# Kernel tuning notes

Measured on AMD Instinct MI355X. Metric: run time of the kernel, lower is better.

The kernel has to match this reference:

```python
import jax, jax.numpy as jnp
import numpy as np

N_NODES = 100000
D = 128
R = 4          # number of edge types
E = 500000     # edges per relation


def setup_inputs() -> dict:
    key = jax.random.key(0)
    ks = jax.random.split(key, 6)
    x = jax.random.normal(ks[0], (N_NODES, D), dtype=jnp.float32)
    src = jax.random.randint(ks[1], (R, E), 0, N_NODES)
    dst = jax.random.randint(ks[2], (R, E), 0, N_NODES)
    # Per-relation SAGEConv (mean) parameters: fc_self, fc_neigh, bias
    scale = 1.0 / np.sqrt(D)
    Wself = jax.random.normal(ks[3], (R, D, D), dtype=jnp.float32) * scale
    Wneigh = jax.random.normal(ks[4], (R, D, D), dtype=jnp.float32) * scale
    b = jnp.zeros((R, D), dtype=jnp.float32)
    return {"x": x, "src": src, "dst": dst, "Wself": Wself, "Wneigh": Wneigh, "b": b}


def reference(x, src, dst, Wself, Wneigh, b):
    """HetGraphLayer with SAGE(mean) convs per relation + mean channel combine.

    x:     [N, D] node features (same node set for all relations)
    src:   [R, E] int source node ids per relation
    dst:   [R, E] int destination node ids per relation
    Wself, Wneigh: [R, D, D]; b: [R, D]
    """
    N = x.shape[0]

    def one_relation(s, d, Ws, Wn, bb):
        msg = x[s]                                                   # [E, D] gather
        summed = jax.ops.segment_sum(msg, d, num_segments=N)         # [N, D] scatter-add
        cnt = jax.ops.segment_sum(jnp.ones(s.shape, x.dtype), d, num_segments=N)
        neigh = summed / jnp.maximum(cnt, 1.0)[:, None]              # mean aggregation
        return x @ Ws + neigh @ Wn + bb                              # SAGEConv(mean)

    rel_embs = jax.vmap(one_relation)(src, dst, Wself, Wneigh, b)    # [R, N, D]
    # ChannelCombine('mean'): average across relation channels
    return rel_embs.mean(axis=0)                                     # [N, D]
```

## Files before the change

### kernel.cpp

```cpp
#include <hip/hip_runtime.h>
#include <hip/hip_bf16.h>
#include <stdint.h>

#define N_NODES 100000
#define DIM 128
#define NREL 4
#define NEDGE 500000
#define M_FLAT (NREL * N_NODES)
#define TOT_E (NREL * NEDGE)
#define BSLOT 1024
#define NBK ((M_FLAT + BSLOT - 1) / BSLOT)
#define CAP 8192
#define CHUNK 4096

typedef __attribute__((ext_vector_type(8))) short short8;
typedef __attribute__((ext_vector_type(4))) float f32x4;
typedef __attribute__((ext_vector_type(2))) float f32x2;

__device__ __forceinline__ unsigned short f2bf(float f) {
  unsigned int u = __float_as_uint(f);
  u += 0x7fffu + ((u >> 16) & 1u);
  return (unsigned short)(u >> 16);
}

__global__ void prep_kernel(const float* __restrict__ Ws, const float* __restrict__ Wn,
                            const float* __restrict__ bv, unsigned short* __restrict__ Wt,
                            float* __restrict__ biasc) {
  int tid = blockIdx.x * 256 + threadIdx.x;
  if (tid < 5 * DIM * DIM) {
    int b = tid / (DIM * DIM);
    int idx = tid - b * DIM * DIM;
    int k = idx >> 7, n = idx & 127;
    float v;
    if (b == 0)
      v = 0.25f * (Ws[idx] + Ws[DIM * DIM + idx] + Ws[2 * DIM * DIM + idx] + Ws[3 * DIM * DIM + idx]);
    else
      v = 0.25f * Wn[(b - 1) * DIM * DIM + idx];
    int ks = k >> 5, kq = (k >> 3) & 3, j = k & 7;
    int ct = n >> 4, lr = n & 15;
    int lane = kq * 16 + lr;
    Wt[((((b * 4 + ks) * 8) + ct) * 64 + lane) * 8 + j] = f2bf(v);
  }
  if (tid < DIM)
    biasc[tid] = 0.25f * (bv[tid] + bv[DIM + tid] + bv[2 * DIM + tid] + bv[3 * DIM + tid]);
}

__global__ void xb_kernel(const float* __restrict__ x, unsigned short* __restrict__ xb) {
  int i = blockIdx.x * 256 + threadIdx.x;
  if (i < N_NODES * DIM / 4) {
    float4 v = ((const float4*)x)[i];
    ushort4 s;
    s.x = f2bf(v.x); s.y = f2bf(v.y); s.z = f2bf(v.z); s.w = f2bf(v.w);
    ((ushort4*)xb)[i] = s;
  }
}

__global__ __launch_bounds__(256) void bscatter_kernel(
    const int* __restrict__ src, const int* __restrict__ dst,
    int* __restrict__ bcnt, unsigned int* __restrict__ gpairs) {
  __shared__ unsigned int buf[CHUNK];
  __shared__ unsigned short barr[CHUNK];
  __shared__ int hist[NBK];
  __shared__ int sbase[NBK];
  __shared__ int lcur[NBK];
  __shared__ int gbase[NBK];
  __shared__ int part[256];
  int tid = threadIdx.x;
  int base = blockIdx.x * CHUNK;
  int m = TOT_E - base; if (m > CHUNK) m = CHUNK;
  for (int i = tid; i < NBK; i += 256) { hist[i] = 0; lcur[i] = 0; }
  __syncthreads();
  unsigned int pk[CHUNK / 256];
  int bk[CHUNK / 256];
#pragma unroll
  for (int k = 0; k < CHUNK / 256; ++k) {
    int i = k * 256 + tid;
    int idx = base + i;
    int b = -1; unsigned int p = 0;
    if (i < m) {
      int r = idx / NEDGE;
      int fl = r * N_NODES + dst[idx];
      b = fl >> 10;
      p = ((unsigned int)(fl & (BSLOT - 1)) << 17) | (unsigned int)src[idx];
      atomicAdd(&hist[b], 1);
    }
    pk[k] = p; bk[k] = b;
  }
  __syncthreads();
  {
    int vA = hist[tid];
    part[tid] = vA;
    __syncthreads();
    for (int o = 1; o < 256; o <<= 1) {
      int u = (tid >= o) ? part[tid - o] : 0;
      __syncthreads();
      part[tid] += u;
      __syncthreads();
    }
    sbase[tid] = part[tid] - vA;
    int totalA = part[255];
    __syncthreads();
    int vB = (256 + tid < NBK) ? hist[256 + tid] : 0;
    part[tid] = vB;
    __syncthreads();
    for (int o = 1; o < 256; o <<= 1) {
      int u = (tid >= o) ? part[tid - o] : 0;
      __syncthreads();
      part[tid] += u;
      __syncthreads();
    }
    if (256 + tid < NBK) sbase[256 + tid] = totalA + part[tid] - vB;
  }
  __syncthreads();
#pragma unroll
  for (int k = 0; k < CHUNK / 256; ++k) {
    if (bk[k] >= 0) {
      int pos = sbase[bk[k]] + atomicAdd(&lcur[bk[k]], 1);
      buf[pos] = pk[k];
      barr[pos] = (unsigned short)bk[k];
    }
  }
  __syncthreads();
  for (int i = tid; i < NBK; i += 256)
    if (hist[i] > 0) gbase[i] = i * CAP + atomicAdd(&bcnt[i], hist[i]) - sbase[i];
  __syncthreads();
  for (int j = tid; j < m; j += 256)
    gpairs[gbase[barr[j]] + j] = buf[j];
}

__global__ __launch_bounds__(256) void bfill_kernel(
    const unsigned int* __restrict__ gpairs, const int* __restrict__ bcnt,
    int* __restrict__ offs, int* __restrict__ ssrc) {
  __shared__ int lcnt[BSLOT];
  __shared__ int lofs[BSLOT];
  __shared__ int lcur[BSLOT];
  __shared__ int part[256];
  int b = blockIdx.x;
  int tid = threadIdx.x;
  int base = b * CAP;
  int cntb = bcnt[b];
  int flBase = b << 10;
  int flCount = M_FLAT - flBase; if (flCount > BSLOT) flCount = BSLOT;
  for (int i = tid; i < BSLOT; i += 256) { lcnt[i] = 0; lcur[i] = 0; }
  __syncthreads();
  for (int j = tid; j < cntb; j += 256)
    atomicAdd(&lcnt[gpairs[base + j] >> 17], 1);
  __syncthreads();
  int vals[4]; int s0 = 0;
#pragma unroll
  for (int k = 0; k < 4; ++k) { vals[k] = lcnt[tid * 4 + k]; s0 += vals[k]; }
  part[tid] = s0;
  __syncthreads();
  for (int o = 1; o < 256; o <<= 1) {
    int u = (tid >= o) ? part[tid - o] : 0;
    __syncthreads();
    part[tid] += u;
    __syncthreads();
  }
  int excl = part[tid] - s0;
#pragma unroll
  for (int k = 0; k < 4; ++k) { lofs[tid * 4 + k] = excl; excl += vals[k]; }
  __syncthreads();
  for (int i = tid; i <= flCount; i += 256)
    offs[b * (BSLOT + 1) + i] = base + ((i < BSLOT) ? lofs[i] : cntb);
  for (int j = tid; j < cntb; j += 256) {
    unsigned int p = gpairs[base + j];
    int li = p >> 17;
    int pos = atomicAdd(&lcur[li], 1);
    ssrc[base + lofs[li] + pos] = (int)(p & 0x1FFFFu);
  }
}

__global__ __launch_bounds__(256) void aggregate_kernel(
    const unsigned int* __restrict__ xb32, const int* __restrict__ ssrc,
    const int* __restrict__ offs, unsigned int* __restrict__ agg32) {
  int lane = threadIdx.x & 63;
  int n = blockIdx.x * 4 + (int)__builtin_amdgcn_readfirstlane(threadIdx.x >> 6);
  if (n >= N_NODES) return;

  int start[NREL], end[NREL];
#pragma unroll
  for (int r = 0; r < NREL; ++r) {
    int fl = r * N_NODES + n;
    int oidx = fl + (fl >> 10);
    start[r] = __builtin_amdgcn_readfirstlane(offs[oidx]);
    end[r] = __builtin_amdgcn_readfirstlane(offs[oidx + 1]);
  }

  unsigned int v[NREL][8];
#pragma unroll
  for (int r = 0; r < NREL; ++r) {
    int s = start[r], m = end[r] - s;
#pragma unroll
    for (int k = 0; k < 8; ++k) {
      int ea = (m > 0) ? (s + ((k < m) ? k : (m - 1))) : 0;
      int idx = ssrc[ea];
      v[r][k] = xb32[((unsigned)idx << 6) | (unsigned)lane];
    }
  }

  f32x2 acc[NREL];
#pragma unroll
  for (int r = 0; r < NREL; ++r) {
    f32x2 a = {0.f, 0.f};
    int m = end[r] - start[r];
#pragma unroll
    for (int k = 0; k < 8; ++k) {
      unsigned int u = (k < m) ? v[r][k] : 0u;
      f32x2 d;
      d.x = __uint_as_float(u << 16);
      d.y = __uint_as_float(u & 0xffff0000u);
      a += d;
    }
    acc[r] = a;
  }

  bool anyTail = ((end[0] - start[0]) > 8) | ((end[1] - start[1]) > 8) |
                 ((end[2] - start[2]) > 8) | ((end[3] - start[3]) > 8);
  if (anyTail) {
#pragma unroll
    for (int r = 0; r < NREL; ++r) {
      for (int e = start[r] + 8; e < end[r]; e += 8) {
        int m = end[r] - e;
        unsigned int w[8];
#pragma unroll
        for (int k = 0; k < 8; ++k) {
          int idx = ssrc[e + ((k < m) ? k : 0)];
          w[k] = xb32[((unsigned)idx << 6) | (unsigned)lane];
        }
#pragma unroll
        for (int k = 0; k < 8; ++k) {
          unsigned int u = (k < m) ? w[k] : 0u;
          f32x2 d;
          d.x = __uint_as_float(u << 16);
          d.y = __uint_as_float(u & 0xffff0000u);
          acc[r] += d;
        }
      }
    }
  }

#pragma unroll
  for (int r = 0; r < NREL; ++r) {
    int c = end[r] - start[r];
    float inv = __builtin_amdgcn_rcpf((float)(c > 0 ? c : 1));
    float lo = acc[r].x * inv, hi = acc[r].y * inv;
    unsigned int packed;
    asm("v_cvt_pk_bf16_f32 %0, %1, %2" : "=v"(packed) : "v"(lo), "v"(hi));
    agg32[((size_t)r * N_NODES + n) * 64 + lane] = packed;
  }
}

__global__ __launch_bounds__(256) void gemm_kernel(
    const unsigned short* __restrict__ xb, const unsigned short* __restrict__ Wt,
    const float* __restrict__ biasc, float* __restrict__ out,
    const unsigned short* __restrict__ agg, int slabBase, int bLo, int bHi, int accum) {
  __shared__ short8 Bs[2048];
  int tid = threadIdx.x;
  int lane = tid & 63;
  int wv = __builtin_amdgcn_readfirstlane(tid >> 6);
  int bandRow = blockIdx.x * 128 + wv * 32;
  int valid = bandRow < N_NODES;
  int ldRow = valid ? bandRow : 0;
  int quad = lane >> 4;
  int lr = lane & 15;
  const short8* Bp = (const short8*)Wt;

  float bias8[8];
#pragma unroll
  for (int ct = 0; ct < 8; ++ct) bias8[ct] = biasc[ct * 16 + lr];

  f32x4 zero = {0.f, 0.f, 0.f, 0.f};
  f32x4 acc[2][8];
#pragma unroll
  for (int rt = 0; rt < 2; ++rt)
#pragma unroll
    for (int ct = 0; ct < 8; ++ct) acc[rt][ct] = zero;

#pragma unroll
  for (int p = 0; p < 8; ++p) Bs[p * 256 + tid] = Bp[(size_t)bLo * 2048 + p * 256 + tid];
  __syncthreads();

  for (int bi = bLo; bi <= bHi; ++bi) {
    const unsigned short* as =
        (bi == 0) ? xb : agg + (size_t)(bi - 1 - slabBase) * N_NODES * DIM;
    const unsigned short* rowp = as + (size_t)(ldRow + lr) * DIM;
    short8 a0[4], a1[4];
#pragma unroll
    for (int ks = 0; ks < 4; ++ks) {
      int k0 = ks * 32 + quad * 8;
      a0[ks] = *(const short8*)(rowp + k0);
      a1[ks] = *(const short8*)(rowp + 16 * DIM + k0);
    }
#pragma unroll
    for (int ks = 0; ks < 4; ++ks) {
#pragma unroll
      for (int ct = 0; ct < 8; ++ct) {
        short8 bf = Bs[(ks * 8 + ct) * 64 + lane];
        acc[0][ct] = __builtin_amdgcn_mfma_f32_16x16x32_bf16(a0[ks], bf, acc[0][ct], 0, 0, 0);
        acc[1][ct] = __builtin_amdgcn_mfma_f32_16x16x32_bf16(a1[ks], bf, acc[1][ct], 0, 0, 0);
      }
    }
    if (bi < bHi) {
      __syncthreads();
#pragma unroll
      for (int p = 0; p < 8; ++p)
        Bs[p * 256 + tid] = Bp[(size_t)(bi + 1) * 2048 + p * 256 + tid];
      __syncthreads();
    }
  }

  if (valid) {
#pragma unroll
    for (int rt = 0; rt < 2; ++rt)
#pragma unroll
      for (int i = 0; i < 4; ++i) {
        int g = bandRow + rt * 16 + quad * 4 + i;
        if (accum == 0) {
#pragma unroll
          for (int ct = 0; ct < 8; ++ct)
            out[(size_t)g * DIM + ct * 16 + lr] = acc[rt][ct][i] + bias8[ct];
        } else {
#pragma unroll
          for (int ct = 0; ct < 8; ++ct)
            out[(size_t)g * DIM + ct * 16 + lr] += acc[rt][ct][i];
        }
      }
  }
}

extern "C" void kernel_launch(void* const* d_in, const int* in_sizes, int n_in,
                              void* d_out, int out_size, void* d_ws, size_t ws_size,
                              hipStream_t stream) {
  const float* x = (const float*)d_in[0];
  const int* src = (const int*)d_in[1];
  const int* dst = (const int*)d_in[2];
  const float* Wself = (const float*)d_in[3];
  const float* Wneigh = (const float*)d_in[4];
  const float* bv = (const float*)d_in[5];
  float* out = (float*)d_out;

  char* ws = (char*)d_ws;
  size_t off = 0;
  int* bcnt = (int*)(ws + off);        off += 2048;
  unsigned short* Wt = (unsigned short*)(ws + off);  off += 5 * DIM * DIM * 2;
  float* biasc = (float*)(ws + off);   off += DIM * 4;
  int* offs = (int*)(ws + off);        off += ((size_t)NBK * (BSLOT + 1) * 4 + 15) & ~15;
  unsigned short* xb = (unsigned short*)(ws + off);  off += (size_t)N_NODES * DIM * 2;
  unsigned int* gpairs = (unsigned int*)(ws + off);  off += (size_t)NBK * CAP * 4;
  int* ssrc = (int*)(ws + off);        off += (size_t)NBK * CAP * 4;
  unsigned short* agg = (unsigned short*)(ws + off);

  hipMemsetAsync(bcnt, 0, 2048, stream);
  xb_kernel<<<(N_NODES * DIM / 4 + 255) / 256, 256, 0, stream>>>(x, xb);
  prep_kernel<<<(5 * DIM * DIM + 255) / 256, 256, 0, stream>>>(Wself, Wneigh, bv, Wt, biasc);
  bscatter_kernel<<<(TOT_E + CHUNK - 1) / CHUNK, 256, 0, stream>>>(src, dst, bcnt, gpairs);
  bfill_kernel<<<NBK, 256, 0, stream>>>(gpairs, bcnt, offs, ssrc);

  int gAgg = (N_NODES + 3) / 4;
  aggregate_kernel<<<gAgg, 256, 0, stream>>>((const unsigned int*)xb, ssrc, offs,
                                             (unsigned int*)agg);
  gemm_kernel<<<(N_NODES + 127) / 128, 256, 0, stream>>>(xb, Wt, biasc, out, agg,
                                                         0, 0, NREL, 0);
}
```

Measured before the change: 304.2 us.

## Fuse preprocessing kernels into one launch and prefetch A tiles in GEMM

Merges the bf16 conversion of x, the weight/bias prep and the edge bucket-scatter into a single block-partitioned kernel, cutting two launches and letting the independent work run concurrently. The scatter chunk size is doubled, which halves the scatter block count but raises shared memory and register use per block. The conversion path now batches eight float4 loads per thread. The GEMM is specialised to a fixed five-slab loop that loads the next slab's A rows while the current slab's MFMAs run.

New measurement: 295.1 us. 3.0% less time.

```diff
diff --git a/kernel.cpp b/kernel.cpp
--- a/kernel.cpp
+++ b/kernel.cpp
@@ -11,7 +11,12 @@
 #define BSLOT 1024
 #define NBK ((M_FLAT + BSLOT - 1) / BSLOT)
 #define CAP 8192
-#define CHUNK 4096
+#define CHUNK 8192
+#define NBSC ((TOT_E + CHUNK - 1) / CHUNK)
+#define NQ (N_NODES * DIM / 4)
+#define XB_BATCH 8
+#define NBXB ((NQ + 256 * XB_BATCH - 1) / (256 * XB_BATCH))
+#define NBPREP ((5 * DIM * DIM + 255) / 256)
 
 typedef __attribute__((ext_vector_type(8))) short short8;
 typedef __attribute__((ext_vector_type(4))) float f32x4;
@@ -23,41 +28,13 @@
   return (unsigned short)(u >> 16);
 }
 
-__global__ void prep_kernel(const float* __restrict__ Ws, const float* __restrict__ Wn,
-                            const float* __restrict__ bv, unsigned short* __restrict__ Wt,
-                            float* __restrict__ biasc) {
-  int tid = blockIdx.x * 256 + threadIdx.x;
-  if (tid < 5 * DIM * DIM) {
-    int b = tid / (DIM * DIM);
-    int idx = tid - b * DIM * DIM;
-    int k = idx >> 7, n = idx & 127;
-    float v;
-    if (b == 0)
-      v = 0.25f * (Ws[idx] + Ws[DIM * DIM + idx] + Ws[2 * DIM * DIM + idx] + Ws[3 * DIM * DIM + idx]);
-    else
-      v = 0.25f * Wn[(b - 1) * DIM * DIM + idx];
-    int ks = k >> 5, kq = (k >> 3) & 3, j = k & 7;
-    int ct = n >> 4, lr = n & 15;
-    int lane = kq * 16 + lr;
-    Wt[((((b * 4 + ks) * 8) + ct) * 64 + lane) * 8 + j] = f2bf(v);
-  }
-  if (tid < DIM)
-    biasc[tid] = 0.25f * (bv[tid] + bv[DIM + tid] + bv[2 * DIM + tid] + bv[3 * DIM + tid]);
-}
-
-__global__ void xb_kernel(const float* __restrict__ x, unsigned short* __restrict__ xb) {
-  int i = blockIdx.x * 256 + threadIdx.x;
-  if (i < N_NODES * DIM / 4) {
-    float4 v = ((const float4*)x)[i];
-    ushort4 s;
-    s.x = f2bf(v.x); s.y = f2bf(v.y); s.z = f2bf(v.z); s.w = f2bf(v.w);
-    ((ushort4*)xb)[i] = s;
-  }
-}
-
-__global__ __launch_bounds__(256) void bscatter_kernel(
+__global__ __launch_bounds__(256) void pre_kernel(
     const int* __restrict__ src, const int* __restrict__ dst,
-    int* __restrict__ bcnt, unsigned int* __restrict__ gpairs) {
+    int* __restrict__ bcnt, unsigned int* __restrict__ gpairs,
+    const float* __restrict__ x, unsigned short* __restrict__ xb,
+    const float* __restrict__ Ws, const float* __restrict__ Wn,
+    const float* __restrict__ bv, unsigned short* __restrict__ Wt,
+    float* __restrict__ biasc) {
   __shared__ unsigned int buf[CHUNK];
   __shared__ unsigned short barr[CHUNK];
   __shared__ int hist[NBK];
@@ -65,67 +42,106 @@
   __shared__ int lcur[NBK];
   __shared__ int gbase[NBK];
   __shared__ int part[256];
+  int bid = blockIdx.x;
   int tid = threadIdx.x;
-  int base = blockIdx.x * CHUNK;
-  int m = TOT_E - base; if (m > CHUNK) m = CHUNK;
-  for (int i = tid; i < NBK; i += 256) { hist[i] = 0; lcur[i] = 0; }
-  __syncthreads();
-  unsigned int pk[CHUNK / 256];
-  int bk[CHUNK / 256];
-#pragma unroll
-  for (int k = 0; k < CHUNK / 256; ++k) {
-    int i = k * 256 + tid;
-    int idx = base + i;
-    int b = -1; unsigned int p = 0;
-    if (i < m) {
-      int r = idx / NEDGE;
-      int fl = r * N_NODES + dst[idx];
-      b = fl >> 10;
-      p = ((unsigned int)(fl & (BSLOT - 1)) << 17) | (unsigned int)src[idx];
-      atomicAdd(&hist[b], 1);
-    }
-    pk[k] = p; bk[k] = b;
-  }
-  __syncthreads();
-  {
-    int vA = hist[tid];
-    part[tid] = vA;
-    __syncthreads();
-    for (int o = 1; o < 256; o <<= 1) {
-      int u = (tid >= o) ? part[tid - o] : 0;
-      __syncthreads();
-      part[tid] += u;
-      __syncthreads();
-    }
-    sbase[tid] = part[tid] - vA;
-    int totalA = part[255];
-    __syncthreads();
-    int vB = (256 + tid < NBK) ? hist[256 + tid] : 0;
-    part[tid] = vB;
-    __syncthreads();
-    for (int o = 1; o < 256; o <<= 1) {
-      int u = (tid >= o) ? part[tid - o] : 0;
-      __syncthreads();
-      part[tid] += u;
-      __syncthreads();
-    }
-    if (256 + tid < NBK) sbase[256 + tid] = totalA + part[tid] - vB;
-  }
-  __syncthreads();
-#pragma unroll
-  for (int k = 0; k < CHUNK / 256; ++k) {
-    if (bk[k] >= 0) {
-      int pos = sbase[bk[k]] + atomicAdd(&lcur[bk[k]], 1);
-      buf[pos] = pk[k];
-      barr[pos] = (unsigned short)bk[k];
-    }
-  }
-  __syncthreads();
-  for (int i = tid; i < NBK; i += 256)
-    if (hist[i] > 0) gbase[i] = i * CAP + atomicAdd(&bcnt[i], hist[i]) - sbase[i];
-  __syncthreads();
-  for (int j = tid; j < m; j += 256)
-    gpairs[gbase[barr[j]] + j] = buf[j];
+
+  if (bid < NBSC) {
+    int base = bid * CHUNK;
+    int m = TOT_E - base; if (m > CHUNK) m = CHUNK;
+    for (int i = tid; i < NBK; i += 256) { hist[i] = 0; lcur[i] = 0; }
+    __syncthreads();
+    unsigned int pk[CHUNK / 256];
+    int bk[CHUNK / 256];
+#pragma unroll
+    for (int k = 0; k < CHUNK / 256; ++k) {
+      int i = k * 256 + tid;
+      int idx = base + i;
+      int b = -1; unsigned int p = 0;
+      if (i < m) {
+        int r = idx / NEDGE;
+        int fl = r * N_NODES + dst[idx];
+        b = fl >> 10;
+        p = ((unsigned int)(fl & (BSLOT - 1)) << 17) | (unsigned int)src[idx];
+        atomicAdd(&hist[b], 1);
+      }
+      pk[k] = p; bk[k] = b;
+    }
+    __syncthreads();
+    {
+      int vA = hist[tid];
+      part[tid] = vA;
+      __syncthreads();
+      for (int o = 1; o < 256; o <<= 1) {
+        int u = (tid >= o) ? part[tid - o] : 0;
+        __syncthreads();
+        part[tid] += u;
+        __syncthreads();
+      }
+      sbase[tid] = part[tid] - vA;
+      int totalA = part[255];
+      __syncthreads();
+      int vB = (256 + tid < NBK) ? hist[256 + tid] : 0;
+      part[tid] = vB;
+      __syncthreads();
+      for (int o = 1; o < 256; o <<= 1) {
+        int u = (tid >= o) ? part[tid - o] : 0;
+        __syncthreads();
+        part[tid] += u;
+        __syncthreads();
+      }
+      if (256 + tid < NBK) sbase[256 + tid] = totalA + part[tid] - vB;
+    }
+    __syncthreads();
+#pragma unroll
+    for (int k = 0; k < CHUNK / 256; ++k) {
+      if (bk[k] >= 0) {
+        int pos = sbase[bk[k]] + atomicAdd(&lcur[bk[k]], 1);
+        buf[pos] = pk[k];
+        barr[pos] = (unsigned short)bk[k];
+      }
+    }
+    __syncthreads();
+    for (int i = tid; i < NBK; i += 256)
+      if (hist[i] > 0) gbase[i] = i * CAP + atomicAdd(&bcnt[i], hist[i]) - sbase[i];
+    __syncthreads();
+    for (int j = tid; j < m; j += 256)
+      gpairs[gbase[barr[j]] + j] = buf[j];
+  } else if (bid < NBSC + NBXB) {
+    int base = (bid - NBSC) * (256 * XB_BATCH);
+    float4 v[XB_BATCH];
+#pragma unroll
+    for (int k = 0; k < XB_BATCH; ++k) {
+      int i = base + k * 256 + tid;
+      if (i < NQ) v[k] = ((const float4*)x)[i];
+    }
+#pragma unroll
+    for (int k = 0; k < XB_BATCH; ++k) {
+      int i = base + k * 256 + tid;
+      if (i < NQ) {
+        ushort4 s;
+        s.x = f2bf(v[k].x); s.y = f2bf(v[k].y); s.z = f2bf(v[k].z); s.w = f2bf(v[k].w);
+        ((ushort4*)xb)[i] = s;
+      }
+    }
+  } else {
+    int t3 = (bid - NBSC - NBXB) * 256 + tid;
+    if (t3 < 5 * DIM * DIM) {
+      int b = t3 / (DIM * DIM);
+      int idx = t3 - b * DIM * DIM;
+      int k = idx >> 7, n = idx & 127;
+      float v;
+      if (b == 0)
+        v = 0.25f * (Ws[idx] + Ws[DIM * DIM + idx] + Ws[2 * DIM * DIM + idx] + Ws[3 * DIM * DIM + idx]);
+      else
+        v = 0.25f * Wn[(b - 1) * DIM * DIM + idx];
+      int ks = k >> 5, kq = (k >> 3) & 3, j = k & 7;
+      int ct = n >> 4, lr = n & 15;
+      int lane = kq * 16 + lr;
+      Wt[((((b * 4 + ks) * 8) + ct) * 64 + lane) * 8 + j] = f2bf(v);
+    }
+    if (t3 < DIM)
+      biasc[t3] = 0.25f * (bv[t3] + bv[DIM + t3] + bv[2 * DIM + t3] + bv[3 * DIM + t3]);
+  }
 }
 
 __global__ __launch_bounds__(256) void bfill_kernel(
@@ -254,7 +270,7 @@
 __global__ __launch_bounds__(256) void gemm_kernel(
     const unsigned short* __restrict__ xb, const unsigned short* __restrict__ Wt,
     const float* __restrict__ biasc, float* __restrict__ out,
-    const unsigned short* __restrict__ agg, int slabBase, int bLo, int bHi, int accum) {
+    const unsigned short* __restrict__ agg) {
   __shared__ short8 Bs[2048];
   int tid = threadIdx.x;
   int lane = tid & 63;
@@ -278,35 +294,48 @@
     for (int ct = 0; ct < 8; ++ct) acc[rt][ct] = zero;
 
 #pragma unroll
-  for (int p = 0; p < 8; ++p) Bs[p * 256 + tid] = Bp[(size_t)bLo * 2048 + p * 256 + tid];
-  __syncthreads();
-
-  for (int bi = bLo; bi <= bHi; ++bi) {
-    const unsigned short* as =
-        (bi == 0) ? xb : agg + (size_t)(bi - 1 - slabBase) * N_NODES * DIM;
-    const unsigned short* rowp = as + (size_t)(ldRow + lr) * DIM;
-    short8 a0[4], a1[4];
+  for (int p = 0; p < 8; ++p) Bs[p * 256 + tid] = Bp[p * 256 + tid];
+  short8 a0c[4], a1c[4];
+  {
+    const unsigned short* rowp = xb + (size_t)(ldRow + lr) * DIM;
 #pragma unroll
     for (int ks = 0; ks < 4; ++ks) {
       int k0 = ks * 32 + quad * 8;
-      a0[ks] = *(const short8*)(rowp + k0);
-      a1[ks] = *(const short8*)(rowp + 16 * DIM + k0);
+      a0c[ks] = *(const short8*)(rowp + k0);
+      a1c[ks] = *(const short8*)(rowp + 16 * DIM + k0);
+    }
+  }
+  __syncthreads();
+
+#pragma unroll
+  for (int bi = 0; bi < 5; ++bi) {
+    short8 a0n[4], a1n[4];
+    if (bi < 4) {
+      const unsigned short* rowp = agg + (size_t)bi * N_NODES * DIM + (size_t)(ldRow + lr) * DIM;
+#pragma unroll
+      for (int ks = 0; ks < 4; ++ks) {
+        int k0 = ks * 32 + quad * 8;
+        a0n[ks] = *(const short8*)(rowp + k0);
+        a1n[ks] = *(const short8*)(rowp + 16 * DIM + k0);
+      }
     }
 #pragma unroll
     for (int ks = 0; ks < 4; ++ks) {
 #pragma unroll
       for (int ct = 0; ct < 8; ++ct) {
         short8 bf = Bs[(ks * 8 + ct) * 64 + lane];
-        acc[0][ct] = __builtin_amdgcn_mfma_f32_16x16x32_bf16(a0[ks], bf, acc[0][ct], 0, 0, 0);
-        acc[1][ct] = __builtin_amdgcn_mfma_f32_16x16x32_bf16(a1[ks], bf, acc[1][ct], 0, 0, 0);
-      }
-    }
-    if (bi < bHi) {
+        acc[0][ct] = __builtin_amdgcn_mfma_f32_16x16x32_bf16(a0c[ks], bf, acc[0][ct], 0, 0, 0);
+        acc[1][ct] = __builtin_amdgcn_mfma_f32_16x16x32_bf16(a1c[ks], bf, acc[1][ct], 0, 0, 0);
+      }
+    }
+    if (bi < 4) {
       __syncthreads();
 #pragma unroll
       for (int p = 0; p < 8; ++p)
         Bs[p * 256 + tid] = Bp[(size_t)(bi + 1) * 2048 + p * 256 + tid];
       __syncthreads();
+#pragma unroll
+      for (int ks = 0; ks < 4; ++ks) { a0c[ks] = a0n[ks]; a1c[ks] = a1n[ks]; }
     }
   }
 
@@ -316,15 +345,9 @@
 #pragma unroll
       for (int i = 0; i < 4; ++i) {
         int g = bandRow + rt * 16 + quad * 4 + i;
-        if (accum == 0) {
-#pragma unroll
-          for (int ct = 0; ct < 8; ++ct)
-            out[(size_t)g * DIM + ct * 16 + lr] = acc[rt][ct][i] + bias8[ct];
-        } else {
-#pragma unroll
-          for (int ct = 0; ct < 8; ++ct)
-            out[(size_t)g * DIM + ct * 16 + lr] += acc[rt][ct][i];
-        }
+#pragma unroll
+        for (int ct = 0; ct < 8; ++ct)
+          out[(size_t)g * DIM + ct * 16 + lr] = acc[rt][ct][i] + bias8[ct];
       }
   }
 }
@@ -352,14 +375,10 @@
   unsigned short* agg = (unsigned short*)(ws + off);
 
   hipMemsetAsync(bcnt, 0, 2048, stream);
-  xb_kernel<<<(N_NODES * DIM / 4 + 255) / 256, 256, 0, stream>>>(x, xb);
-  prep_kernel<<<(5 * DIM * DIM + 255) / 256, 256, 0, stream>>>(Wself, Wneigh, bv, Wt, biasc);
-  bscatter_kernel<<<(TOT_E + CHUNK - 1) / CHUNK, 256, 0, stream>>>(src, dst, bcnt, gpairs);
+  pre_kernel<<<NBSC + NBXB + NBPREP, 256, 0, stream>>>(src, dst, bcnt, gpairs,
+                                                       x, xb, Wself, Wneigh, bv, Wt, biasc);
   bfill_kernel<<<NBK, 256, 0, stream>>>(gpairs, bcnt, offs, ssrc);
-
-  int gAgg = (N_NODES + 3) / 4;
-  aggregate_kernel<<<gAgg, 256, 0, stream>>>((const unsigned int*)xb, ssrc, offs,
-                                             (unsigned int*)agg);
-  gemm_kernel<<<(N_NODES + 127) / 128, 256, 0, stream>>>(xb, Wt, biasc, out, agg,
-                                                         0, 0, NREL, 0);
-}
+  aggregate_kernel<<<(N_NODES + 3) / 4, 256, 0, stream>>>((const unsigned int*)xb, ssrc,
+                                                          offs, (unsigned int*)agg);
+  gemm_kernel<<<(N_NODES + 127) / 128, 256, 0, stream>>>(xb, Wt, biasc, out, agg);
+}
```

## Split aggregation into two relation-pair passes and prefetch GEMM A tiles

Applied to the files above, without the earlier changes.

The aggregate kernel now handles two relations per launch and runs twice, cutting register pressure and the number of in-flight gathers per wave so more waves fit. The GEMM kernel drops the generic slab and accumulate arguments, unrolls the five weight blocks, and loads the next block's A rows into registers before the current block's MFMAs so global latency overlaps compute. The bscatter chunk size is also doubled. The cost is an extra kernel launch, reading the offsets twice, and more live registers in the GEMM.

Measured after the change: 307.7 us. About the same (+1.1%).

```diff
diff --git a/kernel.cpp b/kernel.cpp
--- a/kernel.cpp
+++ b/kernel.cpp
@@ -11,7 +11,7 @@
 #define BSLOT 1024
 #define NBK ((M_FLAT + BSLOT - 1) / BSLOT)
 #define CAP 8192
-#define CHUNK 4096
+#define CHUNK 8192
 
 typedef __attribute__((ext_vector_type(8))) short short8;
 typedef __attribute__((ext_vector_type(4))) float f32x4;
@@ -173,55 +173,54 @@
 
 __global__ __launch_bounds__(256) void aggregate_kernel(
     const unsigned int* __restrict__ xb32, const int* __restrict__ ssrc,
-    const int* __restrict__ offs, unsigned int* __restrict__ agg32) {
+    const int* __restrict__ offs, unsigned int* __restrict__ agg32, int rLo) {
   int lane = threadIdx.x & 63;
   int n = blockIdx.x * 4 + (int)__builtin_amdgcn_readfirstlane(threadIdx.x >> 6);
   if (n >= N_NODES) return;
 
-  int start[NREL], end[NREL];
-#pragma unroll
-  for (int r = 0; r < NREL; ++r) {
-    int fl = r * N_NODES + n;
+  int start[2], end[2];
+#pragma unroll
+  for (int q = 0; q < 2; ++q) {
+    int fl = (rLo + q) * N_NODES + n;
     int oidx = fl + (fl >> 10);
-    start[r] = __builtin_amdgcn_readfirstlane(offs[oidx]);
-    end[r] = __builtin_amdgcn_readfirstlane(offs[oidx + 1]);
-  }
-
-  unsigned int v[NREL][8];
-#pragma unroll
-  for (int r = 0; r < NREL; ++r) {
-    int s = start[r], m = end[r] - s;
+    start[q] = __builtin_amdgcn_readfirstlane(offs[oidx]);
+    end[q] = __builtin_amdgcn_readfirstlane(offs[oidx + 1]);
+  }
+
+  unsigned int v[2][8];
+#pragma unroll
+  for (int q = 0; q < 2; ++q) {
+    int s = start[q], m = end[q] - s;
 #pragma unroll
     for (int k = 0; k < 8; ++k) {
       int ea = (m > 0) ? (s + ((k < m) ? k : (m - 1))) : 0;
       int idx = ssrc[ea];
-      v[r][k] = xb32[((unsigned)idx << 6) | (unsigned)lane];
-    }
-  }
-
-  f32x2 acc[NREL];
-#pragma unroll
-  for (int r = 0; r < NREL; ++r) {
+      v[q][k] = xb32[((unsigned)idx << 6) | (unsigned)lane];
+    }
+  }
+
+  f32x2 acc[2];
+#pragma unroll
+  for (int q = 0; q < 2; ++q) {
     f32x2 a = {0.f, 0.f};
-    int m = end[r] - start[r];
+    int m = end[q] - start[q];
 #pragma unroll
     for (int k = 0; k < 8; ++k) {
-      unsigned int u = (k < m) ? v[r][k] : 0u;
+      unsigned int u = (k < m) ? v[q][k] : 0u;
       f32x2 d;
       d.x = __uint_as_float(u << 16);
       d.y = __uint_as_float(u & 0xffff0000u);
       a += d;
     }
-    acc[r] = a;
-  }
-
-  bool anyTail = ((end[0] - start[0]) > 8) | ((end[1] - start[1]) > 8) |
-                 ((end[2] - start[2]) > 8) | ((end[3] - start[3]) > 8);
+    acc[q] = a;
+  }
+
+  bool anyTail = ((end[0] - start[0]) > 8) | ((end[1] - start[1]) > 8);
   if (anyTail) {
 #pragma unroll
-    for (int r = 0; r < NREL; ++r) {
-      for (int e = start[r] + 8; e < end[r]; e += 8) {
-        int m = end[r] - e;
+    for (int q = 0; q < 2; ++q) {
+      for (int e = start[q] + 8; e < end[q]; e += 8) {
+        int m = end[q] - e;
         unsigned int w[8];
 #pragma unroll
         for (int k = 0; k < 8; ++k) {
@@ -234,27 +233,27 @@
           f32x2 d;
           d.x = __uint_as_float(u << 16);
           d.y = __uint_as_float(u & 0xffff0000u);
-          acc[r] += d;
+          acc[q] += d;
         }
       }
     }
   }
 
 #pragma unroll
-  for (int r = 0; r < NREL; ++r) {
-    int c = end[r] - start[r];
+  for (int q = 0; q < 2; ++q) {
+    int c = end[q] - start[q];
     float inv = __builtin_amdgcn_rcpf((float)(c > 0 ? c : 1));
-    float lo = acc[r].x * inv, hi = acc[r].y * inv;
+    float lo = acc[q].x * inv, hi = acc[q].y * inv;
     unsigned int packed;
     asm("v_cvt_pk_bf16_f32 %0, %1, %2" : "=v"(packed) : "v"(lo), "v"(hi));
-    agg32[((size_t)r * N_NODES + n) * 64 + lane] = packed;
+    agg32[((size_t)(rLo + q) * N_NODES + n) * 64 + lane] = packed;
   }
 }
 
 __global__ __launch_bounds__(256) void gemm_kernel(
     const unsigned short* __restrict__ xb, const unsigned short* __restrict__ Wt,
     const float* __restrict__ biasc, float* __restrict__ out,
-    const unsigned short* __restrict__ agg, int slabBase, int bLo, int bHi, int accum) {
+    const unsigned short* __restrict__ agg) {
   __shared__ short8 Bs[2048];
   int tid = threadIdx.x;
   int lane = tid & 63;
@@ -278,35 +277,48 @@
     for (int ct = 0; ct < 8; ++ct) acc[rt][ct] = zero;
 
 #pragma unroll
-  for (int p = 0; p < 8; ++p) Bs[p * 256 + tid] = Bp[(size_t)bLo * 2048 + p * 256 + tid];
-  __syncthreads();
-
-  for (int bi = bLo; bi <= bHi; ++bi) {
-    const unsigned short* as =
-        (bi == 0) ? xb : agg + (size_t)(bi - 1 - slabBase) * N_NODES * DIM;
-    const unsigned short* rowp = as + (size_t)(ldRow + lr) * DIM;
-    short8 a0[4], a1[4];
+  for (int p = 0; p < 8; ++p) Bs[p * 256 + tid] = Bp[p * 256 + tid];
+  short8 a0c[4], a1c[4];
+  {
+    const unsigned short* rowp = xb + (size_t)(ldRow + lr) * DIM;
 #pragma unroll
     for (int ks = 0; ks < 4; ++ks) {
       int k0 = ks * 32 + quad * 8;
-      a0[ks] = *(const short8*)(rowp + k0);
-      a1[ks] = *(const short8*)(rowp + 16 * DIM + k0);
+      a0c[ks] = *(const short8*)(rowp + k0);
+      a1c[ks] = *(const short8*)(rowp + 16 * DIM + k0);
+    }
+  }
+  __syncthreads();
+
+#pragma unroll
+  for (int bi = 0; bi < 5; ++bi) {
+    short8 a0n[4], a1n[4];
+    if (bi < 4) {
+      const unsigned short* rowp = agg + (size_t)bi * N_NODES * DIM + (size_t)(ldRow + lr) * DIM;
+#pragma unroll
+      for (int ks = 0; ks < 4; ++ks) {
+        int k0 = ks * 32 + quad * 8;
+        a0n[ks] = *(const short8*)(rowp + k0);
+        a1n[ks] = *(const short8*)(rowp + 16 * DIM + k0);
+      }
     }
 #pragma unroll
     for (int ks = 0; ks < 4; ++ks) {
 #pragma unroll
       for (int ct = 0; ct < 8; ++ct) {
         short8 bf = Bs[(ks * 8 + ct) * 64 + lane];
-        acc[0][ct] = __builtin_amdgcn_mfma_f32_16x16x32_bf16(a0[ks], bf, acc[0][ct], 0, 0, 0);
-        acc[1][ct] = __builtin_amdgcn_mfma_f32_16x16x32_bf16(a1[ks], bf, acc[1][ct], 0, 0, 0);
+        acc[0][ct] = __builtin_amdgcn_mfma_f32_16x16x32_bf16(a0c[ks], bf, acc[0][ct], 0, 0, 0);
+        acc[1][ct] = __builtin_amdgcn_mfma_f32_16x16x32_bf16(a1c[ks], bf, acc[1][ct], 0, 0, 0);
       }
     }
-    if (bi < bHi) {
+    if (bi < 4) {
       __syncthreads();
 #pragma unroll
       for (int p = 0; p < 8; ++p)
         Bs[p * 256 + tid] = Bp[(size_t)(bi + 1) * 2048 + p * 256 + tid];
       __syncthreads();
+#pragma unroll
+      for (int ks = 0; ks < 4; ++ks) { a0c[ks] = a0n[ks]; a1c[ks] = a1n[ks]; }
     }
   }
 
@@ -316,15 +328,9 @@
 #pragma unroll
       for (int i = 0; i < 4; ++i) {
         int g = bandRow + rt * 16 + quad * 4 + i;
-        if (accum == 0) {
-#pragma unroll
-          for (int ct = 0; ct < 8; ++ct)
-            out[(size_t)g * DIM + ct * 16 + lr] = acc[rt][ct][i] + bias8[ct];
-        } else {
-#pragma unroll
-          for (int ct = 0; ct < 8; ++ct)
-            out[(size_t)g * DIM + ct * 16 + lr] += acc[rt][ct][i];
-        }
+#pragma unroll
+        for (int ct = 0; ct < 8; ++ct)
+          out[(size_t)g * DIM + ct * 16 + lr] = acc[rt][ct][i] + bias8[ct];
       }
   }
 }
@@ -359,7 +365,8 @@
 
   int gAgg = (N_NODES + 3) / 4;
   aggregate_kernel<<<gAgg, 256, 0, stream>>>((const unsigned int*)xb, ssrc, offs,
-                                             (unsigned int*)agg);
-  gemm_kernel<<<(N_NODES + 127) / 128, 256, 0, stream>>>(xb, Wt, biasc, out, agg,
-                                                         0, 0, NREL, 0);
-}
+                                             (unsigned int*)agg, 0);
+  aggregate_kernel<<<gAgg, 256, 0, stream>>>((const unsigned int*)xb, ssrc, offs,
+                                             (unsigned int*)agg, 2);
+  gemm_kernel<<<(N_NODES + 127) / 128, 256, 0, stream>>>(xb, Wt, biasc, out, agg);
+}
```
